# Optimization experiments

Measured on AMD Instinct MI355X. Metric: run time of the kernel, lower is better.

## Reference

```python
import jax, jax.numpy as jnp
import numpy as np

N = 4194304  # number of 3D points (surfels)
H, W = 1024, 1280


def setup_inputs() -> dict:
    key = jax.random.key(0)
    k1, k2, k3 = jax.random.split(key, 3)
    # camera-frame points: x,y in [-0.5, 0.5], z (depth) in [0.5, 2.5]
    xy = jax.random.uniform(k1, (N, 2), dtype=jnp.float32, minval=-0.5, maxval=0.5)
    z = jax.random.uniform(k2, (N, 1), dtype=jnp.float32, minval=0.5, maxval=2.5)
    points = jnp.concatenate([xy, z], axis=-1)
    colors = jax.random.uniform(k3, (N, 3), dtype=jnp.float32)
    fx = fy = 1000.0
    K = jnp.array([[fx, 0.0, W / 2.0], [0.0, fy, H / 2.0], [0.0, 0.0, 1.0]],
                  dtype=jnp.float32)
    return {"points": points, "colors": colors, "K": K, "height": H, "width": W}


def reference(points, colors, K, height, width):
    # pcd2depth: pinhole projection with rounding
    fx, fy, cx, cy = K[0, 0], K[1, 1], K[0, 2], K[1, 2]
    z = points[:, 2]
    u = jnp.round(fx * points[:, 0] / z + cx).astype(jnp.int32)
    v = jnp.round(fy * points[:, 1] / z + cy).astype(jnp.int32)
    valid = (z > 0) & (u >= 0) & (u < width) & (v >= 0) & (v < height)
    n = points.shape[0]
    npix = height * width
    # sentinel pixel npix for invalid points
    flat = jnp.where(valid, v * width + u, npix)
    # far-to-near overwrite after depth_sort=True)
    order = jnp.argsort(jnp.where(valid, z, jnp.inf))  # ascending depth
    flat_sorted = flat[order]
    ranks = jnp.arange(n, dtype=jnp.int32)
    # per-pixel min rank (rank = position in depth-ascending order)
    win = jnp.full(npix + 1, n, dtype=jnp.int32).at[flat_sorted].min(ranks)
    win = win[:npix]
    has_point = win < n
    winner = order[jnp.minimum(win, n - 1)]  # point index per pixel
    img = jnp.where(has_point[:, None], colors[winner].astype(jnp.float32), 0.0)
    return img.reshape(height, width, 3)
```

## Files before the change

kernel.cpp:

```cpp
#include <hip/hip_runtime.h>
#include <stdint.h>

#define NPTS    4194304
#define IMG_H   1024
#define IMG_W   1280
#define NPIX    (IMG_H * IMG_W)

#define TW      40
#define TH      32
#define TILES_X (IMG_W / TW)
#define TILES_Y (IMG_H / TH)
#define NBINS   (TILES_X * TILES_Y)
#define TPIX    (TW * TH)

#define NBLK    768
#define TPB     256
#define TPB_R   256
#define SEGS_PER_T (NBLK / TPB_R)
#if (NBLK % TPB_R) != 0
#error "NBLK must be a multiple of TPB_R"
#endif

#define CHUNK_Q ((NPTS / 4 + NBLK - 1) / NBLK)
#define CHUNK_P (CHUNK_Q * 4)
#define SSTRIDE CHUNK_P
#define QPT     ((CHUNK_Q + TPB - 1) / TPB)
#define BPT     (NBINS / TPB)

static const unsigned long long KEY_SENTINEL = ~0ULL;
#define KEY47_MASK ((1ULL << 47) - 1)


struct Perm { unsigned short p[NBINS]; };
constexpr Perm make_perm() {
    unsigned short rank[NBINS] = {};
    float score[NBINS] = {};
    for (int i = 0; i < NBINS; ++i) {
        int tx = i % TILES_X, ty = i / TILES_X;
        float du = ((float)tx + 0.5f) * (float)TW - 640.0f;
        float dv = ((float)ty + 0.5f) * (float)TH - 512.0f;
        du /= 640.0f; dv /= 512.0f;
        score[i] = du * du + dv * dv;
        rank[i] = (unsigned short)i;
    }
    for (int i = 1; i < NBINS; ++i) {
        unsigned short key = rank[i];
        float ks = score[key];
        int j = i - 1;
        while (j >= 0 && score[rank[j]] > ks) { rank[j + 1] = rank[j]; --j; }
        rank[j + 1] = key;
    }
    Perm P{};
    for (int i = 0; i < NBINS; ++i) {
        int r = i / 256, k = i % 256;
        int src = (r & 1) ? (r * 256 + (255 - k)) : (r * 256 + k);
        P.p[i] = rank[src];
    }
    return P;
}
__device__ __constant__ Perm c_perm = make_perm();

__device__ __forceinline__ bool project(float x, float y, float z,
                                        float fx, float fy, float cx, float cy,
                                        int& u, int& v) {
    float uf = rintf(fx * x / z + cx);
    float vf = rintf(fy * y / z + cy);
    bool valid = (z > 0.0f) &&
                 (uf >= 0.0f) && (uf < (float)IMG_W) &&
                 (vf >= 0.0f) && (vf < (float)IMG_H);
    u = (int)uf;
    v = (int)vf;
    return valid;
}

__device__ __forceinline__ unsigned int zc_of(float z) {
    unsigned int zb = __float_as_uint(z);
    unsigned int zc = zb - 0x3F000000u;
    if ((int)zc < 0) zc = 0;
    if (zc > 0x1FFFFFFu) zc = 0x1FFFFFFu;
    return zc;
}

__global__ __launch_bounds__(TPB, 3) void pass_bin(
        const float4* __restrict__ pts4, const float* __restrict__ Kmat,
        unsigned int* __restrict__ cnt_off ,
        unsigned long long* __restrict__ grec ,
        int n_quads, int qchunk) {
    __shared__ unsigned long long srec[CHUNK_P];
    __shared__ unsigned int hist[NBINS];
    __shared__ unsigned int cur[NBINS];
    __shared__ unsigned int tsum[TPB];

    int t   = threadIdx.x;
    int blk = blockIdx.x;
#pragma unroll
    for (int i = t; i < NBINS; i += TPB) hist[i] = 0;
    __syncthreads();

    float fx = Kmat[0], cx = Kmat[2];
    float fy = Kmat[4], cy = Kmat[5];

    int q0 = blk * qchunk;
    int q1 = min(n_quads, q0 + qchunk);

    unsigned long long keep[QPT * 4];

#pragma unroll
    for (int qi = 0; qi < QPT; ++qi) {
        int q = q0 + t + qi * TPB;
        bool inb = (q < q1);
        float4 a = {}, b = {}, c = {};
        if (inb) {
            a = pts4[3 * q + 0];
            b = pts4[3 * q + 1];
            c = pts4[3 * q + 2];
        }
        float px[4] = {a.x, a.w, b.z, c.y};
        float py[4] = {a.y, b.x, b.w, c.z};
        float pz[4] = {a.z, b.y, c.x, c.w};
#pragma unroll
        for (int k = 0; k < 4; ++k) {
            unsigned long long kv = ~0ULL;
            int u, v;
            if (inb && project(px[k], py[k], pz[k], fx, fy, cx, cy, u, v)) {
                int tx  = u / TW;
                int bin = (v >> 5) * TILES_X + tx;
                unsigned int pos = (unsigned int)((v & 31) * TW + (u - tx * TW));
                atomicAdd(&hist[bin], 1u);
                kv = ((unsigned long long)bin << 36) |
                     ((unsigned long long)pos << 25) |
                     (unsigned long long)zc_of(pz[k]);
            }
            keep[qi * 4 + k] = kv;
        }
    }
    __syncthreads();

    unsigned int hv[BPT];
    {
        unsigned int s = 0;
#pragma unroll
        for (int j = 0; j < BPT; ++j) { hv[j] = hist[BPT * t + j]; s += hv[j]; }
        tsum[t] = s;
    }
    __syncthreads();
    for (int off = 1; off < TPB; off <<= 1) {
        unsigned int x = (t >= off) ? tsum[t - off] : 0u;
        __syncthreads();
        tsum[t] += x;
        __syncthreads();
    }
    {
        unsigned int run = (t > 0) ? tsum[t - 1] : 0u;
#pragma unroll
        for (int j = 0; j < BPT; ++j) {
            cur[BPT * t + j] = run;
            run += hv[j];
        }
    }
    __syncthreads();

#pragma unroll
    for (int i = t; i < NBINS; i += TPB)
        cnt_off[(size_t)blk * NBINS + i] = (hist[i] << 16) | cur[i];
    __syncthreads();

#pragma unroll
    for (int qi = 0; qi < QPT; ++qi) {
        int q = q0 + t + qi * TPB;
        unsigned int i0 = 4u * (unsigned int)q;
#pragma unroll
        for (int k = 0; k < 4; ++k) {
            unsigned long long kv = keep[qi * 4 + k];
            if (kv != ~0ULL) {
                int bin          = (int)(kv >> 36);
                unsigned int pos = (unsigned int)((kv >> 25) & 0x7FFu);
                unsigned int zc  = (unsigned int)(kv & 0x1FFFFFFu);
                unsigned int slot = atomicAdd(&cur[bin], 1u);
                srec[slot] = ((unsigned long long)pos << 47) |
                             ((unsigned long long)zc << 22) |
                             (unsigned long long)(i0 + (unsigned int)k);
            }
        }
    }
    __syncthreads();

    unsigned int nrec = cur[NBINS - 1];
    unsigned long long* my = grec + (size_t)blk * SSTRIDE;
    for (unsigned int i = t; i < nrec; i += TPB) my[i] = srec[i];
}

__global__ __launch_bounds__(TPB_R) void pass_render(
        const unsigned long long* __restrict__ grec,
        const unsigned int* __restrict__ cnt_off ,
        const float* __restrict__ colors,
        float* __restrict__ out, int npts) {
    __shared__ unsigned long long key[TPIX];

    int t = threadIdx.x;
    int b = c_perm.p[blockIdx.x];

#pragma unroll
    for (int i = t; i < TPIX; i += TPB_R) key[i] = KEY_SENTINEL;

    unsigned int w[SEGS_PER_T];
#pragma unroll
    for (int s = 0; s < SEGS_PER_T; ++s)
        w[s] = cnt_off[(size_t)(t + s * TPB_R) * NBINS + b];
    __syncthreads();

#pragma unroll
    for (int s = 0; s < SEGS_PER_T; ++s) {
        unsigned int cnt = w[s] >> 16;
        unsigned int off = w[s] & 0xFFFFu;
        const unsigned long long* seg =
            grec + (size_t)(t + s * TPB_R) * SSTRIDE + off;
        if ((off & 1u) && cnt) {
            unsigned long long rec = seg[0];
            atomicMin(&key[(unsigned int)(rec >> 47)], rec & KEY47_MASK);
            ++seg; --cnt;
        }
        const ulonglong2* seg2 = (const ulonglong2*)seg;
        unsigned int np = cnt >> 1;
        unsigned int p = 0;
        for (; p + 4 <= np; p += 4) {
            ulonglong2 a  = seg2[p];
            ulonglong2 b2 = seg2[p + 1];
            ulonglong2 c2 = seg2[p + 2];
            ulonglong2 d2 = seg2[p + 3];
            atomicMin(&key[(unsigned int)(a.x  >> 47)], a.x  & KEY47_MASK);
            atomicMin(&key[(unsigned int)(a.y  >> 47)], a.y  & KEY47_MASK);
            atomicMin(&key[(unsigned int)(b2.x >> 47)], b2.x & KEY47_MASK);
            atomicMin(&key[(unsigned int)(b2.y >> 47)], b2.y & KEY47_MASK);
            atomicMin(&key[(unsigned int)(c2.x >> 47)], c2.x & KEY47_MASK);
            atomicMin(&key[(unsigned int)(c2.y >> 47)], c2.y & KEY47_MASK);
            atomicMin(&key[(unsigned int)(d2.x >> 47)], d2.x & KEY47_MASK);
            atomicMin(&key[(unsigned int)(d2.y >> 47)], d2.y & KEY47_MASK);
        }
        for (; p < np; ++p) {
            ulonglong2 a = seg2[p];
            atomicMin(&key[(unsigned int)(a.x >> 47)], a.x & KEY47_MASK);
            atomicMin(&key[(unsigned int)(a.y >> 47)], a.y & KEY47_MASK);
        }
        if (cnt & 1u) {
            unsigned long long rec = seg[cnt - 1];
            atomicMin(&key[(unsigned int)(rec >> 47)], rec & KEY47_MASK);
        }
    }
    __syncthreads();

    int tx = b % TILES_X, ty = b / TILES_X;
#pragma unroll
    for (int i = t; i < TPIX; i += TPB_R) {
        int row = i / TW, col = i - row * TW;
        unsigned long long kk = key[i];
        float r = 0.0f, g = 0.0f, bl = 0.0f;
        if (kk != KEY_SENTINEL) {
            unsigned int idx = (unsigned int)(kk & 0x3FFFFFu);
            if (idx + 1u < (unsigned int)npts) {
                float4 c4 = *(const float4*)(colors + 3u * idx);
                r = c4.x; g = c4.y; bl = c4.z;
            } else {
                r  = colors[3u * idx + 0];
                g  = colors[3u * idx + 1];
                bl = colors[3u * idx + 2];
            }
        }
        size_t gp = (size_t)(ty * TH + row) * IMG_W + (size_t)(tx * TW + col);
        out[3 * gp + 0] = r;
        out[3 * gp + 1] = g;
        out[3 * gp + 2] = bl;
    }
}

__global__ void init_keys_vec(ulonglong2* __restrict__ keys, int n_vec2) {
    int i = blockIdx.x * blockDim.x + threadIdx.x;
    if (i < n_vec2) keys[i] = ulonglong2{~0ULL, ~0ULL};
}

__global__ void scatter_points_pretest(const float4* __restrict__ pts4,
                                       const float* __restrict__ Kmat,
                                       unsigned long long* __restrict__ keys,
                                       int n_quads) {
    int t = blockIdx.x * blockDim.x + threadIdx.x;
    if (t >= n_quads) return;
    float fx = Kmat[0], cx = Kmat[2];
    float fy = Kmat[4], cy = Kmat[5];
    float4 a = pts4[3 * t + 0];
    float4 b = pts4[3 * t + 1];
    float4 c = pts4[3 * t + 2];
    float px[4] = {a.x, a.w, b.z, c.y};
    float py[4] = {a.y, b.x, b.w, c.z};
    float pz[4] = {a.z, b.y, c.x, c.w};
    unsigned int i0 = 4u * (unsigned int)t;
#pragma unroll
    for (int k = 0; k < 4; ++k) {
        int u, v;
        if (!project(px[k], py[k], pz[k], fx, fy, cx, cy, u, v)) continue;
        int pix = v * IMG_W + u;
        unsigned long long key =
            ((unsigned long long)__float_as_uint(pz[k]) << 32) | (i0 + k);
        if (key < keys[pix]) atomicMin(&keys[pix], key);
    }
}

__global__ void resolve_pixels4(const unsigned long long* __restrict__ keys,
                                const float* __restrict__ colors,
                                float* __restrict__ out, int n_quads) {
    int t = blockIdx.x * blockDim.x + threadIdx.x;
    if (t >= n_quads) return;
    int base = 4 * t;
    ulonglong2 k01 = *(const ulonglong2*)(keys + base);
    ulonglong2 k23 = *(const ulonglong2*)(keys + base + 2);
    unsigned long long kk[4] = {k01.x, k01.y, k23.x, k23.y};
    float c[12];
#pragma unroll
    for (int j = 0; j < 4; ++j) {
        float r = 0.0f, g = 0.0f, b = 0.0f;
        if (kk[j] != KEY_SENTINEL) {
            unsigned int idx = (unsigned int)(kk[j] & 0xFFFFFFFFu);
            r = colors[3 * idx + 0];
            g = colors[3 * idx + 1];
            b = colors[3 * idx + 2];
        }
        c[3 * j + 0] = r; c[3 * j + 1] = g; c[3 * j + 2] = b;
    }
    float4* o = (float4*)(out + 3 * (size_t)base);
    o[0] = float4{c[0], c[1], c[2],  c[3]};
    o[1] = float4{c[4], c[5], c[6],  c[7]};
    o[2] = float4{c[8], c[9], c[10], c[11]};
}

extern "C" void kernel_launch(void* const* d_in, const int* in_sizes, int n_in,
                              void* d_out, int out_size, void* d_ws, size_t ws_size,
                              hipStream_t stream) {
    const float4* pts4  = (const float4*)d_in[0];
    const float* colors = (const float*)d_in[1];
    const float* Kmat   = (const float*)d_in[2];
    float* out = (float*)d_out;

    int n       = in_sizes[0] / 3;
    int n_quads = n / 4;
    int qchunk  = (n_quads + NBLK - 1) / NBLK;

    char* ws = (char*)d_ws;
    size_t off = 0;
    auto alloc = [&](size_t bytes) {
        char* p = ws + off;
        off += (bytes + 63) & ~(size_t)63;
        return p;
    };
    unsigned int*       cnt_off = (unsigned int*)alloc((size_t)NBLK * NBINS * 4);
    unsigned long long* grec =
        (unsigned long long*)alloc((size_t)NBLK * SSTRIDE * 8);

    if (qchunk <= CHUNK_Q && ws_size >= off) {
        pass_bin<<<NBLK, TPB, 0, stream>>>(pts4, Kmat, cnt_off, grec,
                                           n_quads, qchunk);
        pass_render<<<NBINS, TPB_R, 0, stream>>>(grec, cnt_off, colors, out, n);
    } else {
        unsigned long long* keys = (unsigned long long*)d_ws;
        const int B = 256;
        int n_vec2 = NPIX / 2;
        init_keys_vec<<<(n_vec2 + B - 1) / B, B, 0, stream>>>(
            (ulonglong2*)keys, n_vec2);
        scatter_points_pretest<<<(n_quads + B - 1) / B, B, 0, stream>>>(
            pts4, Kmat, keys, n_quads);
        int npix_quads = NPIX / 4;
        resolve_pixels4<<<(npix_quads + B - 1) / B, B, 0, stream>>>(
            keys, colors, out, npix_quads);
    }
}
```

Baseline: 163.2 us.

## Merge histogram into packed cursor array, use wave-shuffle scan, raise binning occupancy

The binning kernel drops the separate histogram array and reuses the cursor array for counts. Offsets are packed with counts in the high 16 bits, so the slot atomics mask to the low 16 bits. The block-wide Hillis-Steele scan through shared memory becomes a wave-level shuffle scan plus a small cross-wave sum, cutting many barriers. NBLK rises to 1024, making per-block chunks smaller and launch bounds allow 4 blocks per CU, aiming for higher occupancy from less LDS per block. The render pass now merges more segments per tile, which may add cost there.

```diff
diff --git a/kernel.cpp b/kernel.cpp
--- a/kernel.cpp
+++ b/kernel.cpp
@@ -13,7 +13,7 @@
 #define NBINS   (TILES_X * TILES_Y)
 #define TPIX    (TW * TH)
 
-#define NBLK    768
+#define NBLK    1024
 #define TPB     256
 #define TPB_R   256
 #define SEGS_PER_T (NBLK / TPB_R)
@@ -81,20 +81,19 @@
     return zc;
 }
 
-__global__ __launch_bounds__(TPB, 3) void pass_bin(
+__global__ __launch_bounds__(TPB, 4) void pass_bin(
         const float4* __restrict__ pts4, const float* __restrict__ Kmat,
         unsigned int* __restrict__ cnt_off ,
         unsigned long long* __restrict__ grec ,
         int n_quads, int qchunk) {
     __shared__ unsigned long long srec[CHUNK_P];
-    __shared__ unsigned int hist[NBINS];
     __shared__ unsigned int cur[NBINS];
-    __shared__ unsigned int tsum[TPB];
+    __shared__ unsigned int wsum[TPB / 64];
 
     int t   = threadIdx.x;
     int blk = blockIdx.x;
 #pragma unroll
-    for (int i = t; i < NBINS; i += TPB) hist[i] = 0;
+    for (int i = t; i < NBINS; i += TPB) cur[i] = 0;
     __syncthreads();
 
     float fx = Kmat[0], cx = Kmat[2];
@@ -126,7 +125,7 @@
                 int tx  = u / TW;
                 int bin = (v >> 5) * TILES_X + tx;
                 unsigned int pos = (unsigned int)((v & 31) * TW + (u - tx * TW));
-                atomicAdd(&hist[bin], 1u);
+                atomicAdd(&cur[bin], 1u);
                 kv = ((unsigned long long)bin << 36) |
                      ((unsigned long long)pos << 25) |
                      (unsigned long long)zc_of(pz[k]);
@@ -137,32 +136,35 @@
     __syncthreads();
 
     unsigned int hv[BPT];
-    {
-        unsigned int s = 0;
-#pragma unroll
-        for (int j = 0; j < BPT; ++j) { hv[j] = hist[BPT * t + j]; s += hv[j]; }
-        tsum[t] = s;
-    }
-    __syncthreads();
-    for (int off = 1; off < TPB; off <<= 1) {
-        unsigned int x = (t >= off) ? tsum[t - off] : 0u;
-        __syncthreads();
-        tsum[t] += x;
-        __syncthreads();
-    }
-    {
-        unsigned int run = (t > 0) ? tsum[t - 1] : 0u;
-#pragma unroll
-        for (int j = 0; j < BPT; ++j) {
-            cur[BPT * t + j] = run;
-            run += hv[j];
-        }
+    unsigned int s = 0;
+#pragma unroll
+    for (int j = 0; j < BPT; ++j) { hv[j] = cur[BPT * t + j]; s += hv[j]; }
+
+    unsigned int lane = (unsigned int)(t & 63);
+    unsigned int wid  = (unsigned int)(t >> 6);
+    unsigned int x = s;
+#pragma unroll
+    for (int d = 1; d < 64; d <<= 1) {
+        unsigned int y = __shfl_up(x, d, 64);
+        if (lane >= (unsigned int)d) x += y;
+    }
+    if (lane == 63u) wsum[wid] = x;
+    __syncthreads();
+    unsigned int wpre = 0;
+#pragma unroll
+    for (int wj = 0; wj < TPB / 64; ++wj)
+        if ((unsigned int)wj < wid) wpre += wsum[wj];
+    unsigned int run = wpre + x - s;
+#pragma unroll
+    for (int j = 0; j < BPT; ++j) {
+        cur[BPT * t + j] = (hv[j] << 16) | run;
+        run += hv[j];
     }
     __syncthreads();
 
 #pragma unroll
     for (int i = t; i < NBINS; i += TPB)
-        cnt_off[(size_t)blk * NBINS + i] = (hist[i] << 16) | cur[i];
+        cnt_off[(size_t)blk * NBINS + i] = cur[i];
     __syncthreads();
 
 #pragma unroll
@@ -176,7 +178,7 @@
                 int bin          = (int)(kv >> 36);
                 unsigned int pos = (unsigned int)((kv >> 25) & 0x7FFu);
                 unsigned int zc  = (unsigned int)(kv & 0x1FFFFFFu);
-                unsigned int slot = atomicAdd(&cur[bin], 1u);
+                unsigned int slot = atomicAdd(&cur[bin], 1u) & 0xFFFFu;
                 srec[slot] = ((unsigned long long)pos << 47) |
                              ((unsigned long long)zc << 22) |
                              (unsigned long long)(i0 + (unsigned int)k);
@@ -185,7 +187,7 @@
     }
     __syncthreads();
 
-    unsigned int nrec = cur[NBINS - 1];
+    unsigned int nrec = cur[NBINS - 1] & 0xFFFFu;
     unsigned long long* my = grec + (size_t)blk * SSTRIDE;
     for (unsigned int i = t; i < nrec; i += TPB) my[i] = srec[i];
 }
```

Result: no change. 164.1 us (+0.5%).
